# Performance work log

Measured on AMD Instinct MI355X. Metric: run time of the kernel, lower is better.

## Reference

```python
import jax, jax.numpy as jnp
import numpy as np

B, S, D = 2, 2048, 2048
H, H_KV, HD = 8, 1, 256   # attention heads, kv heads, head_dim
N_REP = H // H_KV


def setup_inputs() -> dict:
    key = jax.random.key(0)
    ks = jax.random.split(key, 8)
    std = 1.0 / np.sqrt(D)
    return {
        "hidden_states": jax.random.normal(ks[0], (B, S, D), dtype=jnp.float32),
        "attention_mask": jnp.zeros((B, 1, S, S), dtype=jnp.float32),
        "cos": jax.random.uniform(ks[1], (B, S, HD), dtype=jnp.float32),
        "sin": jax.random.uniform(ks[2], (B, S, HD), dtype=jnp.float32),
        "Wq": jax.random.normal(ks[3], (D, H * HD), dtype=jnp.float32) * std,
        "Wk": jax.random.normal(ks[4], (D, H_KV * HD), dtype=jnp.float32) * std,
        "Wv": jax.random.normal(ks[5], (D, H_KV * HD), dtype=jnp.float32) * std,
        "Wo": jax.random.normal(ks[6], (H * HD, D), dtype=jnp.float32) * std,
    }


def _rotate_half(x):
    x1, x2 = jnp.split(x, 2, axis=-1)
    return jnp.concatenate((-x2, x1), axis=-1)


def reference(hidden_states, attention_mask, cos, sin, Wq, Wk, Wv, Wo):
    b, s, _ = hidden_states.shape
    # projections -> [b, heads, s, hd]
    q = (hidden_states @ Wq).reshape(b, s, H, HD).transpose(0, 2, 1, 3)
    k = (hidden_states @ Wk).reshape(b, s, H_KV, HD).transpose(0, 2, 1, 3)
    v = (hidden_states @ Wv).reshape(b, s, H_KV, HD).transpose(0, 2, 1, 3)
    # RoPE (unsqueeze_dim=1)
    c = cos[:, None, :, :]
    sn = sin[:, None, :, :]
    q = q * c + _rotate_half(q) * sn
    k = k * c + _rotate_half(k) * sn
    # GQA: repeat kv heads
    k = jnp.repeat(k, N_REP, axis=1)
    v = jnp.repeat(v, N_REP, axis=1)
    # attention
    scores = jnp.einsum("bhqd,bhkd->bhqk", q, k) / jnp.sqrt(jnp.float32(HD))
    scores = scores + attention_mask[:, :, :, :k.shape[2]]
    attn_weights = jax.nn.softmax(scores.astype(jnp.float32), axis=-1).astype(q.dtype)
    # dropout p=0.0 -> identity
    out = jnp.einsum("bhqk,bhkd->bhqd", attn_weights, v)
    out = out.transpose(0, 2, 1, 3).reshape(b, s, H * HD)
    out = out @ Wo
    return out, attn_weights
```

## Files before the change

### kernel.cpp

```cpp
#include <hip/hip_runtime.h>
#include <hip/hip_bf16.h>

typedef float f32x4 __attribute__((ext_vector_type(4)));
typedef short short8 __attribute__((ext_vector_type(8)));
typedef unsigned int uint2v __attribute__((ext_vector_type(2)));

#define DI __device__ __forceinline__

DI unsigned short f2bf(float f) {
  unsigned int u = __float_as_uint(f);
  u += 0x7fffu + ((u >> 16) & 1u);
  return (unsigned short)(u >> 16);
}

DI unsigned int packbf(float a, float b) {
  return (unsigned int)f2bf(a) | ((unsigned int)f2bf(b) << 16);
}

DI void gload16(const unsigned short* g, unsigned short* l) {
  __builtin_amdgcn_global_load_lds((const __attribute__((address_space(1))) void*)g,
                                   (__attribute__((address_space(3))) void*)l, 16, 0, 0);
}

__global__ void cvt_bf16_kernel(const float* __restrict__ src,
                                unsigned short* __restrict__ dst, long n) {
  long i = ((long)blockIdx.x * blockDim.x + threadIdx.x) * 8;
  if (i >= n) return;
  float4 a = *(const float4*)(src + i);
  float4 b = *(const float4*)(src + i + 4);
  short8 v;
  v[0] = f2bf(a.x); v[1] = f2bf(a.y); v[2] = f2bf(a.z); v[3] = f2bf(a.w);
  v[4] = f2bf(b.x); v[5] = f2bf(b.y); v[6] = f2bf(b.z); v[7] = f2bf(b.w);
  *(short8*)(dst + i) = v;
}

__global__ void transpose_cvt_kernel(const float* __restrict__ src,
                                     unsigned short* __restrict__ dst,
                                     int ldsrc, int lddst, long sBatch, long dBatch) {
  __shared__ float tile[32][33];
  const float* s = src + (long)blockIdx.z * sBatch;
  unsigned short* d = dst + (long)blockIdx.z * dBatch;
  int c0 = blockIdx.x * 32, r0 = blockIdx.y * 32;
  int tx = threadIdx.x, ty = threadIdx.y;
#pragma unroll
  for (int k = 0; k < 4; k++)
    tile[ty + 8 * k][tx] = s[(long)(r0 + ty + 8 * k) * ldsrc + c0 + tx];
  __syncthreads();
#pragma unroll
  for (int k = 0; k < 4; k++)
    d[(long)(c0 + ty + 8 * k) * lddst + r0 + tx] = f2bf(tile[tx][ty + 8 * k]);
}

__global__ void transpose_v_kernel(const float* __restrict__ qkv,
                                   unsigned short* __restrict__ VtC) {
  __shared__ float tile[32][33];
  int b = blockIdx.z;
  int d0 = blockIdx.x * 32, s0 = blockIdx.y * 32;
  int tx = threadIdx.x, ty = threadIdx.y;
  const float* s = qkv + (long)b * 2048 * 2560 + 2304;
#pragma unroll
  for (int k = 0; k < 4; k++)
    tile[ty + 8 * k][tx] = s[(long)(s0 + ty + 8 * k) * 2560 + d0 + tx];
  __syncthreads();
  unsigned short* d = VtC + (long)b * 524288 + (long)(s0 >> 5) * 8192;
#pragma unroll
  for (int k = 0; k < 4; k++) {
    int dd = d0 + ty + 8 * k;
    d[dd * 32 + (tx ^ (((dd >> 1) & 3) << 3))] = f2bf(tile[tx][ty + 8 * k]);
  }
}

__global__ void rope_kernel(const float* __restrict__ qkv, const float* __restrict__ cs,
                            const float* __restrict__ sn, unsigned short* __restrict__ Qb,
                            unsigned short* __restrict__ Ksw) {
  int bid = blockIdx.x;
  int hp = bid % 9;
  int bs = bid / 9;
  int d = threadIdx.x;
  long row = (long)bs * 2560 + hp * 256;
  float x = qkv[row + d];
  float o = (d < 128) ? -qkv[row + d + 128] : qkv[row + d - 128];
  long ci = (long)bs * 256 + d;
  float r = x * cs[ci] + o * sn[ci];
  unsigned short v = f2bf(r);
  if (hp < 8) {
    int b = bs >> 11, s = bs & 2047;
    Qb[((long)(b * 8 + hp) * 2048 + s) * 256 + d] = v;
  } else {
    Ksw[(long)bs * 256 + (d ^ ((bs & 7) << 3))] = v;
  }
}

template <bool AF32, bool CBF16>
__launch_bounds__(256)
__global__ void gemm_bt_kernel(const void* __restrict__ Av,
                               const unsigned short* __restrict__ Btg,
                               void* __restrict__ Cv,
                               int K, int lda, int ldb, int ldc,
                               int zShift, long aBatch, long bBatch, long cBatch, long cHead) {
  __shared__ unsigned short Asm_[128 * 32];
  __shared__ unsigned short Bsm_[128 * 32];
  int z = blockIdx.z;
  int zb = z >> zShift, zh = z - (zb << zShift);
  const unsigned short* Bt = Btg + (long)zb * bBatch;
  const unsigned short* A16 = (const unsigned short*)Av + (long)z * aBatch;
  const float* A32 = (const float*)Av + (long)z * aBatch;
  int nwg = gridDim.x * gridDim.y;
  int bid = blockIdx.y * gridDim.x + blockIdx.x;
  int qq = nwg >> 3;
  int swz = (bid & 7) * qq + (bid >> 3);
  int m0 = (swz / gridDim.x) * 128, n0 = (swz % gridDim.x) * 128;
  int tid = threadIdx.x, w = tid >> 6, lane = tid & 63, c = lane & 15, t = lane >> 4;
  int wm = w >> 1, wn = w & 1;
  f32x4 zero4 = {0.f, 0.f, 0.f, 0.f};
  f32x4 acc[4][4];
#pragma unroll
  for (int i = 0; i < 4; i++)
#pragma unroll
    for (int j = 0; j < 4; j++) acc[i][j] = zero4;

  for (int kt = 0; kt < K; kt += 32) {
    if constexpr (!AF32) {
#pragma unroll
      for (int jj = 0; jj < 2; jj++) {
        int slot = (w * 2 + jj) * 64 + lane;
        int r = slot >> 2, g = slot & 3;
        int gs = g ^ ((r >> 1) & 3);
        gload16(A16 + (long)(m0 + r) * lda + kt + gs * 8, Asm_ + slot * 8);
      }
    } else {
#pragma unroll
      for (int jj = 0; jj < 2; jj++) {
        int slot = jj * 256 + tid;
        int r = slot >> 2, g = slot & 3;
        int gs = g ^ ((r >> 1) & 3);
        const float* p = A32 + (long)(m0 + r) * lda + kt + gs * 8;
        float4 x = *(const float4*)p;
        float4 y = *(const float4*)(p + 4);
        short8 v;
        v[0] = f2bf(x.x); v[1] = f2bf(x.y); v[2] = f2bf(x.z); v[3] = f2bf(x.w);
        v[4] = f2bf(y.x); v[5] = f2bf(y.y); v[6] = f2bf(y.z); v[7] = f2bf(y.w);
        *(short8*)(Asm_ + slot * 8) = v;
      }
    }
#pragma unroll
    for (int jj = 0; jj < 2; jj++) {
      int slot = (w * 2 + jj) * 64 + lane;
      int r = slot >> 2, g = slot & 3;
      int gs = g ^ ((r >> 1) & 3);
      gload16(Bt + (long)(n0 + r) * ldb + kt + gs * 8, Bsm_ + slot * 8);
    }
    __syncthreads();
    short8 af[4], bfg[4];
#pragma unroll
    for (int mi = 0; mi < 4; mi++) {
      int r = wm * 64 + mi * 16 + c;
      af[mi] = *(const short8*)(Asm_ + r * 32 + ((t ^ ((r >> 1) & 3)) * 8));
    }
#pragma unroll
    for (int ni = 0; ni < 4; ni++) {
      int r = wn * 64 + ni * 16 + c;
      bfg[ni] = *(const short8*)(Bsm_ + r * 32 + ((t ^ ((r >> 1) & 3)) * 8));
    }
#pragma unroll
    for (int mi = 0; mi < 4; mi++)
#pragma unroll
      for (int ni = 0; ni < 4; ni++)
        acc[mi][ni] = __builtin_amdgcn_mfma_f32_16x16x32_bf16(af[mi], bfg[ni], acc[mi][ni], 0, 0, 0);
    __syncthreads();
  }
  long cOff = (long)zb * cBatch + zh * cHead;
#pragma unroll
  for (int mi = 0; mi < 4; mi++) {
#pragma unroll
    for (int j = 0; j < 4; j++) {
      int row = m0 + wm * 64 + mi * 16 + t * 4 + j;
#pragma unroll
      for (int ni = 0; ni < 4; ni++) {
        int col = n0 + wn * 64 + ni * 16 + c;
        float v = acc[mi][ni][j];
        long idx = cOff + (long)row * ldc + col;
        if constexpr (CBF16) ((unsigned short*)Cv)[idx] = f2bf(v);
        else ((float*)Cv)[idx] = v;
      }
    }
  }
}

#define KC 32
__launch_bounds__(512, 4)
__global__ void attn_fused_kernel(const unsigned short* __restrict__ Qb,
                                  const unsigned short* __restrict__ Ksw,
                                  const unsigned short* __restrict__ VtC,
                                  const float* __restrict__ mask,
                                  float* __restrict__ attnW,
                                  unsigned short* __restrict__ attnO) {
  __shared__ unsigned short Ksm[2][KC * 256];
  __shared__ unsigned short Vsm[2][256 * KC];
  __shared__ unsigned short Pt[4][16 * 32];
  __shared__ float red[8][16];
  const int id = blockIdx.x;
  const int sw = (id & 7) * 64 + (id >> 3);
  const int qblk = sw & 31, bh = sw >> 5;
  const int b = bh >> 3;
  const int tid = threadIdx.x, w = tid >> 6, lane = tid & 63;
  const int c = lane & 15, t = lane >> 4;
  const int s = w & 3, h = w >> 2;
  const int q0 = qblk * 64 + s * 16;
  const int kh = 16 * h;
  const float scale = 0.0625f;

  short8 qf[8];
  {
    const unsigned short* Qrow = Qb + ((long)bh * 2048 + q0 + c) * 256 + t * 8;
#pragma unroll
    for (int ks = 0; ks < 8; ks++) qf[ks] = *(const short8*)(Qrow + ks * 32);
  }

  const unsigned short* Kg = Ksw + (long)b * 524288;
  const unsigned short* Vg = VtC + (long)b * 524288;
  const float* mrow = mask + (long)b * 4194304 + (long)(q0 + c) * 2048 + kh + t * 4;

  float lp = 0.f;

#pragma unroll
  for (int i = 0; i < 2; i++) {
    int slot = i * 512 + tid;
    gload16(Kg + slot * 8, Ksm[0] + slot * 8);
  }
  f32x4 mv = *(const f32x4*)(mrow);
  for (int kc = 0; kc < 64; kc++) {
    int cur = kc & 1;
    asm volatile("s_barrier" ::: "memory");
    f32x4 mvn;
    if (kc < 63) {
      const unsigned short* src = Kg + (long)(kc + 1) * 8192;
#pragma unroll
      for (int i = 0; i < 2; i++) {
        int slot = i * 512 + tid;
        gload16(src + slot * 8, Ksm[cur ^ 1] + slot * 8);
      }
      mvn = *(const f32x4*)(mrow + (kc + 1) * 32);
      asm volatile("s_waitcnt vmcnt(3)" ::: "memory");
    } else {
      asm volatile("s_waitcnt vmcnt(0)" ::: "memory");
    }
    __builtin_amdgcn_sched_barrier(0);
    f32x4 a0 = {0.f, 0.f, 0.f, 0.f};
    __builtin_amdgcn_s_setprio(1);
#pragma unroll
    for (int ks = 0; ks < 8; ks++) {
      int g0 = ((ks * 4 + t) ^ (c & 7)) * 8;
      short8 kf = *(const short8*)(Ksm[cur] + (kh + c) * 256 + g0);
      a0 = __builtin_amdgcn_mfma_f32_16x16x32_bf16(kf, qf[ks], a0, 0, 0, 0);
    }
    __builtin_amdgcn_s_setprio(0);
#pragma unroll
    for (int j = 0; j < 4; j++) lp += __expf(a0[j] * scale + mv[j]);
    mv = mvn;
  }
  lp += __shfl_xor(lp, 16);
  lp += __shfl_xor(lp, 32);
  if (t == 0) red[w][c] = lp;
  __syncthreads();
  float rinv = 1.0f / (red[s][c] + red[4 + s][c]);

  float* aWrow = attnW + (long)bh * 4194304 + (long)(q0 + c) * 2048 + kh + t * 4;
  unsigned short* myPt = &Pt[s][0];
  const int psw = ((c >> 1) & 3) << 3;
  f32x4 accO[8];
#pragma unroll
  for (int i = 0; i < 8; i++) accO[i] = (f32x4){0.f, 0.f, 0.f, 0.f};

#pragma unroll
  for (int i = 0; i < 2; i++) {
    int slot = i * 512 + tid;
    gload16(Kg + slot * 8, Ksm[0] + slot * 8);
    gload16(Vg + slot * 8, Vsm[0] + slot * 8);
  }
  mv = *(const f32x4*)(mrow);
  for (int kc = 0; kc < 64; kc++) {
    int cur = kc & 1;
    asm volatile("s_barrier" ::: "memory");
    f32x4 mvn;
    if (kc < 63) {
      const unsigned short* ksrc = Kg + (long)(kc + 1) * 8192;
      const unsigned short* vsrc = Vg + (long)(kc + 1) * 8192;
#pragma unroll
      for (int i = 0; i < 2; i++) {
        int slot = i * 512 + tid;
        gload16(ksrc + slot * 8, Ksm[cur ^ 1] + slot * 8);
        gload16(vsrc + slot * 8, Vsm[cur ^ 1] + slot * 8);
      }
      mvn = *(const f32x4*)(mrow + (kc + 1) * 32);
      asm volatile("s_waitcnt vmcnt(5)" ::: "memory");
    } else {
      asm volatile("s_waitcnt vmcnt(0)" ::: "memory");
    }
    __builtin_amdgcn_sched_barrier(0);
    f32x4 a0 = {0.f, 0.f, 0.f, 0.f};
    __builtin_amdgcn_s_setprio(1);
#pragma unroll
    for (int ks = 0; ks < 8; ks++) {
      int g0 = ((ks * 4 + t) ^ (c & 7)) * 8;
      short8 kf = *(const short8*)(Ksm[cur] + (kh + c) * 256 + g0);
      a0 = __builtin_amdgcn_mfma_f32_16x16x32_bf16(kf, qf[ks], a0, 0, 0, 0);
    }
    __builtin_amdgcn_s_setprio(0);
    f32x4 p;
#pragma unroll
    for (int j = 0; j < 4; j++) p[j] = __expf(a0[j] * scale + mv[j]) * rinv;
    mv = mvn;
    *(f32x4*)(aWrow + kc * 32) = p;
    uint2v pw;
    pw[0] = packbf(p[0], p[1]); pw[1] = packbf(p[2], p[3]);
    *(uint2v*)(myPt + c * 32 + ((kh + t * 4) ^ psw)) = pw;
    asm volatile("s_waitcnt lgkmcnt(0)" ::: "memory");
    __builtin_amdgcn_s_barrier();
    __builtin_amdgcn_sched_barrier(0);
    short8 pa = *(const short8*)(myPt + c * 32 + ((t * 8) ^ psw));
    __builtin_amdgcn_s_setprio(1);
#pragma unroll
    for (int di = 0; di < 8; di++) {
      int d = (8 * h + di) * 16 + c;
      short8 vf = *(const short8*)(Vsm[cur] + d * 32 + ((t * 8) ^ psw));
      accO[di] = __builtin_amdgcn_mfma_f32_16x16x32_bf16(pa, vf, accO[di], 0, 0, 0);
    }
    __builtin_amdgcn_s_setprio(0);
  }
  long obase = ((long)b * 2048 + q0 + t * 4) * 2048 + (bh & 7) * 256 + h * 128 + c;
#pragma unroll
  for (int di = 0; di < 8; di++)
#pragma unroll
    for (int j = 0; j < 4; j++)
      attnO[obase + (long)j * 2048 + di * 16] = f2bf(accO[di][j]);
}

extern "C" void kernel_launch(void* const* d_in, const int* in_sizes, int n_in,
                              void* d_out, int out_size, void* d_ws, size_t ws_size,
                              hipStream_t stream) {
  const float* hidden = (const float*)d_in[0];
  const float* mask = (const float*)d_in[1];
  const float* cosb = (const float*)d_in[2];
  const float* sinb = (const float*)d_in[3];
  const float* Wq = (const float*)d_in[4];
  const float* Wk = (const float*)d_in[5];
  const float* Wv = (const float*)d_in[6];
  const float* Wo = (const float*)d_in[7];
  float* out = (float*)d_out;
  float* attnW = out + 8388608;

  char* ws = (char*)d_ws;
  unsigned short* hidB  = (unsigned short*)(ws + 0);
  unsigned short* WqkvT = (unsigned short*)(ws + 16777216);
  unsigned short* WoT   = (unsigned short*)(ws + 27262976);
  float*          qkv   = (float*)(ws + 35651584);
  unsigned short* Qb    = (unsigned short*)(ws + 77594624);
  unsigned short* Ksw   = (unsigned short*)(ws + 94371840);
  unsigned short* VtC   = (unsigned short*)(ws + 96468992);
  unsigned short* attnO = (unsigned short*)(ws + 98566144);

  cvt_bf16_kernel<<<4096, 256, 0, stream>>>(hidden, hidB, 8388608L);
  transpose_cvt_kernel<<<dim3(64, 64, 1), dim3(32, 8), 0, stream>>>(Wq, WqkvT, 2048, 2048, 0, 0);
  transpose_cvt_kernel<<<dim3(8, 64, 1), dim3(32, 8), 0, stream>>>(Wk, WqkvT + (long)2048 * 2048, 256, 2048, 0, 0);
  transpose_cvt_kernel<<<dim3(8, 64, 1), dim3(32, 8), 0, stream>>>(Wv, WqkvT + (long)2304 * 2048, 256, 2048, 0, 0);
  transpose_cvt_kernel<<<dim3(64, 64, 1), dim3(32, 8), 0, stream>>>(Wo, WoT, 2048, 2048, 0, 0);
  gemm_bt_kernel<false, false><<<dim3(20, 32, 1), 256, 0, stream>>>(
      hidB, WqkvT, qkv, 2048, 2048, 2048, 2560, 0, 0, 0, 0, 0);
  rope_kernel<<<36864, 256, 0, stream>>>(qkv, cosb, sinb, Qb, Ksw);
  transpose_v_kernel<<<dim3(8, 64, 2), dim3(32, 8), 0, stream>>>(qkv, VtC);
  attn_fused_kernel<<<512, 512, 0, stream>>>(Qb, Ksw, VtC, mask, attnW, attnO);
  gemm_bt_kernel<false, false><<<dim3(16, 32, 1), 256, 0, stream>>>(
      attnO, WoT, out, 2048, 2048, 2048, 2048, 0, 0, 0, 0, 0);
}
```

Before: 384.4 us.

## Software-pipeline PV matmul one chunk behind QK to drop a per-iteration barrier

Double-buffers the P tile in shared memory and defers each chunk's P·V MFMAs to the next iteration, so the QK^T and softmax work of chunk kc overlaps the PV work of chunk kc-1. This removes the second block barrier per loop iteration. V loads are shifted to fetch the current chunk into the current buffer, and a final PV step runs after the loop. The buffer reuse now relies on the single top-of-loop barrier and on vmcnt accounting, which risks races if those counts are off.

```diff
diff --git a/kernel.cpp b/kernel.cpp
--- a/kernel.cpp
+++ b/kernel.cpp
@@ -197,7 +197,7 @@
                                   unsigned short* __restrict__ attnO) {
   __shared__ unsigned short Ksm[2][KC * 256];
   __shared__ unsigned short Vsm[2][256 * KC];
-  __shared__ unsigned short Pt[4][16 * 32];
+  __shared__ unsigned short Pt[2][4][16 * 32];
   __shared__ float red[8][16];
   const int id = blockIdx.x;
   const int sw = (id & 7) * 64 + (id >> 3);
@@ -266,7 +266,6 @@
   float rinv = 1.0f / (red[s][c] + red[4 + s][c]);
 
   float* aWrow = attnW + (long)bh * 4194304 + (long)(q0 + c) * 2048 + kh + t * 4;
-  unsigned short* myPt = &Pt[s][0];
   const int psw = ((c >> 1) & 3) << 3;
   f32x4 accO[8];
 #pragma unroll
@@ -276,7 +275,6 @@
   for (int i = 0; i < 2; i++) {
     int slot = i * 512 + tid;
     gload16(Kg + slot * 8, Ksm[0] + slot * 8);
-    gload16(Vg + slot * 8, Vsm[0] + slot * 8);
   }
   mv = *(const f32x4*)(mrow);
   for (int kc = 0; kc < 64; kc++) {
@@ -285,17 +283,23 @@
     f32x4 mvn;
     if (kc < 63) {
       const unsigned short* ksrc = Kg + (long)(kc + 1) * 8192;
-      const unsigned short* vsrc = Vg + (long)(kc + 1) * 8192;
+      const unsigned short* vsrc = Vg + (long)kc * 8192;
 #pragma unroll
       for (int i = 0; i < 2; i++) {
         int slot = i * 512 + tid;
         gload16(ksrc + slot * 8, Ksm[cur ^ 1] + slot * 8);
-        gload16(vsrc + slot * 8, Vsm[cur ^ 1] + slot * 8);
+        gload16(vsrc + slot * 8, Vsm[cur] + slot * 8);
       }
       mvn = *(const f32x4*)(mrow + (kc + 1) * 32);
       asm volatile("s_waitcnt vmcnt(5)" ::: "memory");
     } else {
-      asm volatile("s_waitcnt vmcnt(0)" ::: "memory");
+      const unsigned short* vsrc = Vg + (long)kc * 8192;
+#pragma unroll
+      for (int i = 0; i < 2; i++) {
+        int slot = i * 512 + tid;
+        gload16(vsrc + slot * 8, Vsm[cur] + slot * 8);
+      }
+      asm volatile("s_waitcnt vmcnt(2)" ::: "memory");
     }
     __builtin_amdgcn_sched_barrier(0);
     f32x4 a0 = {0.f, 0.f, 0.f, 0.f};
@@ -314,19 +318,31 @@
     *(f32x4*)(aWrow + kc * 32) = p;
     uint2v pw;
     pw[0] = packbf(p[0], p[1]); pw[1] = packbf(p[2], p[3]);
-    *(uint2v*)(myPt + c * 32 + ((kh + t * 4) ^ psw)) = pw;
+    *(uint2v*)(&Pt[cur][s][0] + c * 32 + ((kh + t * 4) ^ psw)) = pw;
+    if (kc >= 1) {
+      short8 pa = *(const short8*)(&Pt[cur ^ 1][s][0] + c * 32 + ((t * 8) ^ psw));
+      __builtin_amdgcn_s_setprio(1);
+#pragma unroll
+      for (int di = 0; di < 8; di++) {
+        int d = (8 * h + di) * 16 + c;
+        short8 vf = *(const short8*)(Vsm[cur ^ 1] + d * 32 + ((t * 8) ^ psw));
+        accO[di] = __builtin_amdgcn_mfma_f32_16x16x32_bf16(pa, vf, accO[di], 0, 0, 0);
+      }
+      __builtin_amdgcn_s_setprio(0);
+    }
     asm volatile("s_waitcnt lgkmcnt(0)" ::: "memory");
-    __builtin_amdgcn_s_barrier();
-    __builtin_amdgcn_sched_barrier(0);
-    short8 pa = *(const short8*)(myPt + c * 32 + ((t * 8) ^ psw));
-    __builtin_amdgcn_s_setprio(1);
+  }
+  asm volatile("s_waitcnt vmcnt(0)" ::: "memory");
+  __builtin_amdgcn_s_barrier();
+  __builtin_amdgcn_sched_barrier(0);
+  {
+    short8 pa = *(const short8*)(&Pt[1][s][0] + c * 32 + ((t * 8) ^ psw));
 #pragma unroll
     for (int di = 0; di < 8; di++) {
       int d = (8 * h + di) * 16 + c;
-      short8 vf = *(const short8*)(Vsm[cur] + d * 32 + ((t * 8) ^ psw));
+      short8 vf = *(const short8*)(Vsm[1] + d * 32 + ((t * 8) ^ psw));
       accO[di] = __builtin_amdgcn_mfma_f32_16x16x32_bf16(pa, vf, accO[di], 0, 0, 0);
     }
-    __builtin_amdgcn_s_setprio(0);
   }
   long obase = ((long)b * 2048 + q0 + t * 4) * 2048 + (bh & 7) * 256 + h * 128 + c;
 #pragma unroll
```

New measurement: 379.8 us. Within noise of the previous version (-1.2%).
